# Kernel tuning notes

Measured on AMD Instinct MI355X. Metric: run time of the kernel, lower is better.

The kernel has to match this reference:

```python
import jax, jax.numpy as jnp
import numpy as np

B, S, E, H = 2, 2048, 1024, 16
HD = E // H


def setup_inputs() -> dict:
    key = jax.random.key(0)
    k1, k2, k3, k4 = jax.random.split(key, 4)
    x = jax.random.normal(k1, (B, S, E), dtype=jnp.float32)
    # nn.Linear(E, 3E, bias=False): weight shape (3E, E), y = x @ W.T
    w_qkv = jax.random.normal(k2, (3 * E, E), dtype=jnp.float32) * (E ** -0.5)
    w_proj = jax.random.normal(k3, (E, E), dtype=jnp.float32) * (E ** -0.5)
    b_proj = jax.random.normal(k4, (E,), dtype=jnp.float32) * 0.02
    return {"x": x, "w_qkv": w_qkv, "w_proj": w_proj, "b_proj": b_proj}


def reference(x, w_qkv, w_proj, b_proj):
    b, s, e = x.shape
    hd = e // H
    qkv = x @ w_qkv.T                                   # (B,S,3E)
    qkv = qkv.reshape(b, s, H, 3, hd)                   # matches view(B,S,H,3*hd).chunk(3,-1)
    q = jnp.transpose(qkv[..., 0, :], (0, 2, 1, 3))      # (B,H,S,hd)
    k = jnp.transpose(qkv[..., 1, :], (0, 2, 1, 3))
    v = jnp.transpose(qkv[..., 2, :], (0, 2, 1, 3))
    scale = hd ** -0.5
    scores = jnp.einsum('bhqd,bhkd->bhqk', q, k) * scale  # (B,H,S,S)
    causal = jnp.tril(jnp.ones((s, s), dtype=bool))
    scores = jnp.where(causal, scores, jnp.float32(-jnp.inf))
    probs = jax.nn.softmax(scores, axis=-1)
    out = jnp.einsum('bhqk,bhkd->bhqd', probs, v)        # (B,H,S,hd)
    out = jnp.transpose(out, (0, 2, 1, 3)).reshape(b, s, e)
    return out @ w_proj.T + b_proj
```

## Files before the change

kernel.cpp:

```cpp
#include <hip/hip_runtime.h>
#include <hip/hip_bf16.h>

#define B_    2
#define S_    2048
#define E_    1024
#define H_    16
#define HD_   64
#define M_    (B_ * S_)
#define QKVN  (3 * E_)

typedef __attribute__((ext_vector_type(8))) short  short8;
typedef __attribute__((ext_vector_type(4))) float  f32x4;

static __device__ __forceinline__ unsigned short f2bf(float f) {
  union { float f; unsigned int u; } c; c.f = f;
  unsigned int u = c.u;
  return (unsigned short)((u + 0x7fffu + ((u >> 16) & 1u)) >> 16);
}

static __device__ __forceinline__ void gload16(unsigned short* lds,
                                               const unsigned short* g) {
  __builtin_amdgcn_global_load_lds(
      (__attribute__((address_space(1))) void*)g,
      (__attribute__((address_space(3))) void*)lds, 16, 0, 0);
}

__global__ __launch_bounds__(256) void cvt_f32_to_bf16(
    const float* __restrict__ in, unsigned short* __restrict__ out, int n4) {
  int i = blockIdx.x * 256 + threadIdx.x;
  if (i < n4) {
    float4 v = reinterpret_cast<const float4*>(in)[i];
    ushort4 r;
    r.x = f2bf(v.x); r.y = f2bf(v.y); r.z = f2bf(v.z); r.w = f2bf(v.w);
    reinterpret_cast<ushort4*>(out)[i] = r;
  }
}

template <int BF16_OUT>
__global__ __launch_bounds__(256) void gemm_bt(
    const unsigned short* __restrict__ A, const unsigned short* __restrict__ Bt,
    void* __restrict__ Cout, const float* __restrict__ bias,
    int M, int N, int K, int ldc) {
  __shared__ alignas(16) unsigned short lds_a[128 * 64];
  __shared__ alignas(16) unsigned short lds_b[128 * 64];
  const int t  = threadIdx.x;
  const int w  = t >> 6, l = t & 63, g = l >> 4, lr = l & 15;
  const int bm = blockIdx.y * 128, bn = blockIdx.x * 128;
  const int wr = (w >> 1) * 64,  wc = (w & 1) * 64;

  f32x4 acc[4][4] = {};

  for (int k0 = 0; k0 < K; k0 += 64) {
    __syncthreads();
#pragma unroll
    for (int i = 0; i < 4; i++) {
      const int pass = w * 4 + i;
      const int r = pass * 8 + (l >> 3);
      const int c = (l & 7) ^ (r & 7);
      gload16(lds_a + pass * 512, A + (size_t)(bm + r) * K + k0 + c * 8);
      gload16(lds_b + pass * 512, Bt + (size_t)(bn + r) * K + k0 + c * 8);
    }
    __syncthreads();

    short8 af[4][2], bfr[4][2];
#pragma unroll
    for (int m = 0; m < 4; m++) {
      const int R = wr + m * 16 + lr;
#pragma unroll
      for (int kk = 0; kk < 2; kk++)
        af[m][kk] = *(const short8*)((const char*)lds_a +
            ((R * 128 + kk * 64 + g * 16) ^ ((R & 7) << 4)));
    }
#pragma unroll
    for (int n = 0; n < 4; n++) {
      const int R = wc + n * 16 + lr;
#pragma unroll
      for (int kk = 0; kk < 2; kk++)
        bfr[n][kk] = *(const short8*)((const char*)lds_b +
            ((R * 128 + kk * 64 + g * 16) ^ ((R & 7) << 4)));
    }
#pragma unroll
    for (int m = 0; m < 4; m++)
#pragma unroll
      for (int n = 0; n < 4; n++) {
        acc[m][n] = __builtin_amdgcn_mfma_f32_16x16x32_bf16(
            af[m][0], bfr[n][0], acc[m][n], 0, 0, 0);
        acc[m][n] = __builtin_amdgcn_mfma_f32_16x16x32_bf16(
            af[m][1], bfr[n][1], acc[m][n], 0, 0, 0);
      }
  }

#pragma unroll
  for (int m = 0; m < 4; m++)
#pragma unroll
    for (int n = 0; n < 4; n++)
#pragma unroll
      for (int j = 0; j < 4; j++) {
        const int row = bm + wr + m * 16 + g * 4 + j;
        const int col = bn + wc + n * 16 + lr;
        const float v = acc[m][n][j];
        if constexpr (BF16_OUT) {
          ((unsigned short*)Cout)[(size_t)row * ldc + col] = f2bf(v);
        } else {
          ((float*)Cout)[(size_t)row * ldc + col] = v + bias[col];
        }
      }
}

__global__ __launch_bounds__(256) void attn_fwd(
    const unsigned short* __restrict__ qkv, unsigned short* __restrict__ attn_out) {
  __shared__ alignas(16) unsigned short lds_k[64 * 64];
  __shared__ alignas(16) unsigned short lds_vt[64 * 64];
  __shared__ alignas(16) unsigned short lds_p[4][32 * 64];

  const int t = threadIdx.x;
  const int w = t >> 6, l = t & 63, g = l >> 4, lr = l & 15;
  const int bid = blockIdx.x;
  const int bh = bid & 31, b = bh >> 4, h = bh & 15;
  const int rr = bid >> 5;
  const int bx = (rr < 8) ? rr : 23 - rr;
  const int q0 = bx * 128;
  const int qw = q0 + w * 32;
  const unsigned short* base = qkv + (size_t)b * S_ * QKVN + h * (3 * HD_);

  short8 qf[2][2];
#pragma unroll
  for (int m = 0; m < 2; m++) {
    const unsigned short* qp = base + (size_t)(qw + m * 16 + lr) * QKVN + g * 8;
    qf[m][0] = *(const short8*)qp;
    qf[m][1] = *(const short8*)(qp + 32);
  }

  f32x4 o[2][4] = {};
  float m_r[2][4], l_r[2][4];
#pragma unroll
  for (int m = 0; m < 2; m++)
#pragma unroll
    for (int j = 0; j < 4; j++) { m_r[m][j] = -3.0e38f; l_r[m][j] = 0.f; }

  const int numt = 2 * bx + 2;
  for (int kt = 0; kt < numt; kt++) {
    const int k0 = kt * 64;
    __syncthreads();
#pragma unroll
    for (int p = 0; p < 2; p++) {
      const int r  = p * 32 + (t >> 3);
      const int kc = t & 7;
      const unsigned short* kp = base + (size_t)(k0 + r) * QKVN + HD_ + kc * 8;
      short8 kv8 = *(const short8*)kp;
      *(short8*)((char*)lds_k + ((r * 128 + kc * 16) ^ ((r & 7) << 4))) = kv8;
      short8 vv8 = *(const short8*)(kp + HD_);
#pragma unroll
      for (int j = 0; j < 8; j++) {
        const int d = kc * 8 + j;
        const int swz = ((d & 7) ^ ((d >> 3) & 7)) << 4;
        *(unsigned short*)((char*)lds_vt + ((d * 128 + r * 2) ^ swz)) =
            (unsigned short)vv8[j];
      }
    }
    __syncthreads();

    f32x4 s[2][4];
    __builtin_amdgcn_s_setprio(1);
#pragma unroll
    for (int n = 0; n < 4; n++) {
      const int R = n * 16 + lr;
      short8 b0 = *(const short8*)((const char*)lds_k +
          ((R * 128 + g * 16) ^ ((R & 7) << 4)));
      short8 b1 = *(const short8*)((const char*)lds_k +
          ((R * 128 + 64 + g * 16) ^ ((R & 7) << 4)));
#pragma unroll
      for (int m = 0; m < 2; m++) {
        f32x4 z = {};
        z = __builtin_amdgcn_mfma_f32_16x16x32_bf16(qf[m][0], b0, z, 0, 0, 0);
        z = __builtin_amdgcn_mfma_f32_16x16x32_bf16(qf[m][1], b1, z, 0, 0, 0);
        s[m][n] = z;
      }
    }
    __builtin_amdgcn_s_setprio(0);

    if (k0 + 63 > qw) {
#pragma unroll
      for (int m = 0; m < 2; m++)
#pragma unroll
        for (int n = 0; n < 4; n++) {
          const int kvc = k0 + n * 16 + lr;
#pragma unroll
          for (int j = 0; j < 4; j++) {
            const int qrow = qw + m * 16 + g * 4 + j;
            if (kvc > qrow) s[m][n][j] = -3.0e38f;
          }
        }
    }

#pragma unroll
    for (int m = 0; m < 2; m++) {
#pragma unroll
      for (int j = 0; j < 4; j++) {
        const float v0 = s[m][0][j] * 0.125f, v1 = s[m][1][j] * 0.125f;
        const float v2 = s[m][2][j] * 0.125f, v3 = s[m][3][j] * 0.125f;
        float mx = fmaxf(fmaxf(v0, v1), fmaxf(v2, v3));
#pragma unroll
        for (int dd = 8; dd; dd >>= 1) mx = fmaxf(mx, __shfl_xor(mx, dd, 16));
        const float mn = fmaxf(m_r[m][j], mx);
        const float c  = __expf(m_r[m][j] - mn);
        m_r[m][j] = mn;
        const float e0 = __expf(v0 - mn), e1 = __expf(v1 - mn);
        const float e2 = __expf(v2 - mn), e3 = __expf(v3 - mn);
        float sum = (e0 + e1) + (e2 + e3);
#pragma unroll
        for (int dd = 8; dd; dd >>= 1) sum += __shfl_xor(sum, dd, 16);
        l_r[m][j] = l_r[m][j] * c + sum;
#pragma unroll
        for (int dt = 0; dt < 4; dt++) o[m][dt][j] *= c;
        const int row = m * 16 + g * 4 + j;
        const int sw  = (row & 7) << 4;
        char* pb = (char*)lds_p[w];
        *(unsigned short*)(pb + ((row * 128 +      lr * 2) ^ sw)) = f2bf(e0);
        *(unsigned short*)(pb + ((row * 128 + 32 + lr * 2) ^ sw)) = f2bf(e1);
        *(unsigned short*)(pb + ((row * 128 + 64 + lr * 2) ^ sw)) = f2bf(e2);
        *(unsigned short*)(pb + ((row * 128 + 96 + lr * 2) ^ sw)) = f2bf(e3);
      }
    }
    __asm__ volatile("s_waitcnt lgkmcnt(0)" ::: "memory");

    __builtin_amdgcn_s_setprio(1);
#pragma unroll
    for (int m = 0; m < 2; m++) {
      const int prow = m * 16 + lr;
      const int psw  = (prow & 7) << 4;
      short8 pf0 = *(const short8*)((const char*)lds_p[w] +
          ((prow * 128 + g * 16) ^ psw));
      short8 pf1 = *(const short8*)((const char*)lds_p[w] +
          ((prow * 128 + 64 + g * 16) ^ psw));
#pragma unroll
      for (int dt = 0; dt < 4; dt++) {
        const int R = dt * 16 + lr;
        const int vsw = ((R & 7) ^ ((R >> 3) & 7)) << 4;
        short8 vf0 = *(const short8*)((const char*)lds_vt +
            ((R * 128 + g * 16) ^ vsw));
        short8 vf1 = *(const short8*)((const char*)lds_vt +
            ((R * 128 + 64 + g * 16) ^ vsw));
        o[m][dt] = __builtin_amdgcn_mfma_f32_16x16x32_bf16(pf0, vf0, o[m][dt], 0, 0, 0);
        o[m][dt] = __builtin_amdgcn_mfma_f32_16x16x32_bf16(pf1, vf1, o[m][dt], 0, 0, 0);
      }
    }
    __builtin_amdgcn_s_setprio(0);
  }

  unsigned short* outp = attn_out + (size_t)b * S_ * E_ + h * HD_;
#pragma unroll
  for (int m = 0; m < 2; m++)
#pragma unroll
    for (int j = 0; j < 4; j++) {
      const float inv = 1.0f / l_r[m][j];
      const int qrow = qw + m * 16 + g * 4 + j;
#pragma unroll
      for (int dt = 0; dt < 4; dt++)
        outp[(size_t)qrow * E_ + dt * 16 + lr] = f2bf(o[m][dt][j] * inv);
    }
}

extern "C" void kernel_launch(void* const* d_in, const int* in_sizes, int n_in,
                              void* d_out, int out_size, void* d_ws, size_t ws_size,
                              hipStream_t stream) {
  (void)in_sizes; (void)n_in; (void)out_size; (void)ws_size;
  const float* x      = (const float*)d_in[0];
  const float* w_qkv  = (const float*)d_in[1];
  const float* w_proj = (const float*)d_in[2];
  const float* b_proj = (const float*)d_in[3];
  float* out = (float*)d_out;

  unsigned short* x_bf     = (unsigned short*)d_ws;
  unsigned short* wqkv_bf  = x_bf    + (size_t)M_ * E_;
  unsigned short* wproj_bf = wqkv_bf + (size_t)QKVN * E_;
  unsigned short* qkv_bf   = wproj_bf + (size_t)E_ * E_;
  unsigned short* attn_bf  = qkv_bf  + (size_t)M_ * QKVN;

  int n4;
  n4 = M_ * E_ / 4;
  cvt_f32_to_bf16<<<(n4 + 255) / 256, 256, 0, stream>>>(x, x_bf, n4);
  n4 = QKVN * E_ / 4;
  cvt_f32_to_bf16<<<(n4 + 255) / 256, 256, 0, stream>>>(w_qkv, wqkv_bf, n4);
  n4 = E_ * E_ / 4;
  cvt_f32_to_bf16<<<(n4 + 255) / 256, 256, 0, stream>>>(w_proj, wproj_bf, n4);

  gemm_bt<1><<<dim3(QKVN / 128, M_ / 128), 256, 0, stream>>>(
      x_bf, wqkv_bf, (void*)qkv_bf, nullptr, M_, QKVN, E_, QKVN);

  attn_fwd<<<dim3(512), 256, 0, stream>>>(qkv_bf, attn_bf);

  gemm_bt<0><<<dim3(E_ / 128, M_ / 128), 256, 0, stream>>>(
      attn_bf, wproj_bf, (void*)out, b_proj, M_, E_, E_, E_);
}
```

Measured before the change: 244.1 us.

## Prefetch next K/V tile into registers, skip masked warp tiles, use DPP reductions

```diff
diff --git a/kernel.cpp b/kernel.cpp
--- a/kernel.cpp
+++ b/kernel.cpp
@@ -23,6 +23,29 @@
   __builtin_amdgcn_global_load_lds(
       (__attribute__((address_space(1))) void*)g,
       (__attribute__((address_space(3))) void*)lds, 16, 0, 0);
+}
+
+static __device__ __forceinline__ float dpp_max16(float x) {
+  x = fmaxf(x, __int_as_float(__builtin_amdgcn_update_dpp(
+          0, __float_as_int(x), 0xB1, 0xF, 0xF, true)));
+  x = fmaxf(x, __int_as_float(__builtin_amdgcn_update_dpp(
+          0, __float_as_int(x), 0x4E, 0xF, 0xF, true)));
+  x = fmaxf(x, __int_as_float(__builtin_amdgcn_update_dpp(
+          0, __float_as_int(x), 0x141, 0xF, 0xF, true)));
+  x = fmaxf(x, __int_as_float(__builtin_amdgcn_update_dpp(
+          0, __float_as_int(x), 0x140, 0xF, 0xF, true)));
+  return x;
+}
+static __device__ __forceinline__ float dpp_sum16(float x) {
+  x += __int_as_float(__builtin_amdgcn_update_dpp(
+          0, __float_as_int(x), 0xB1, 0xF, 0xF, true));
+  x += __int_as_float(__builtin_amdgcn_update_dpp(
+          0, __float_as_int(x), 0x4E, 0xF, 0xF, true));
+  x += __int_as_float(__builtin_amdgcn_update_dpp(
+          0, __float_as_int(x), 0x141, 0xF, 0xF, true));
+  x += __int_as_float(__builtin_amdgcn_update_dpp(
+          0, __float_as_int(x), 0x140, 0xF, 0xF, true));
+  return x;
 }
 
 __global__ __launch_bounds__(256) void cvt_f32_to_bf16(
@@ -114,7 +137,7 @@
   __shared__ alignas(16) unsigned short lds_p[4][32 * 64];
 
   const int t = threadIdx.x;
-  const int w = t >> 6, l = t & 63, g = l >> 4, lr = l & 15;
+  const int w = t >> 6, l = t & 63, g = (l >> 4) & 3, lr = l & 15;
   const int bid = blockIdx.x;
   const int bh = bid & 31, b = bh >> 4, h = bh & 15;
   const int rr = bid >> 5;
@@ -139,113 +162,129 @@
     for (int j = 0; j < 4; j++) { m_r[m][j] = -3.0e38f; l_r[m][j] = 0.f; }
 
   const int numt = 2 * bx + 2;
+  const int r_st = t >> 3;
+  const int kc   = t & 7;
+
+  short8 kreg[2], vreg[2];
+#pragma unroll
+  for (int p = 0; p < 2; p++) {
+    const unsigned short* kp =
+        base + (size_t)(p * 32 + r_st) * QKVN + HD_ + kc * 8;
+    kreg[p] = *(const short8*)kp;
+    vreg[p] = *(const short8*)(kp + HD_);
+  }
+
   for (int kt = 0; kt < numt; kt++) {
     const int k0 = kt * 64;
-    __syncthreads();
 #pragma unroll
     for (int p = 0; p < 2; p++) {
-      const int r  = p * 32 + (t >> 3);
-      const int kc = t & 7;
-      const unsigned short* kp = base + (size_t)(k0 + r) * QKVN + HD_ + kc * 8;
-      short8 kv8 = *(const short8*)kp;
-      *(short8*)((char*)lds_k + ((r * 128 + kc * 16) ^ ((r & 7) << 4))) = kv8;
-      short8 vv8 = *(const short8*)(kp + HD_);
+      const int r = p * 32 + r_st;
+      *(short8*)((char*)lds_k + ((r * 128 + kc * 16) ^ ((r & 7) << 4))) = kreg[p];
 #pragma unroll
       for (int j = 0; j < 8; j++) {
         const int d = kc * 8 + j;
         const int swz = ((d & 7) ^ ((d >> 3) & 7)) << 4;
         *(unsigned short*)((char*)lds_vt + ((d * 128 + r * 2) ^ swz)) =
-            (unsigned short)vv8[j];
+            (unsigned short)vreg[p][j];
+      }
+    }
+    if (kt + 1 < numt) {
+#pragma unroll
+      for (int p = 0; p < 2; p++) {
+        const unsigned short* kp =
+            base + (size_t)(k0 + 64 + p * 32 + r_st) * QKVN + HD_ + kc * 8;
+        kreg[p] = *(const short8*)kp;
+        vreg[p] = *(const short8*)(kp + HD_);
       }
     }
     __syncthreads();
 
-    f32x4 s[2][4];
-    __builtin_amdgcn_s_setprio(1);
-#pragma unroll
-    for (int n = 0; n < 4; n++) {
-      const int R = n * 16 + lr;
-      short8 b0 = *(const short8*)((const char*)lds_k +
-          ((R * 128 + g * 16) ^ ((R & 7) << 4)));
-      short8 b1 = *(const short8*)((const char*)lds_k +
-          ((R * 128 + 64 + g * 16) ^ ((R & 7) << 4)));
+    if (k0 <= qw + 31) {
+      f32x4 s[2][4];
+      __builtin_amdgcn_s_setprio(1);
+#pragma unroll
+      for (int n = 0; n < 4; n++) {
+        const int R = n * 16 + lr;
+        short8 b0 = *(const short8*)((const char*)lds_k +
+            ((R * 128 + g * 16) ^ ((R & 7) << 4)));
+        short8 b1 = *(const short8*)((const char*)lds_k +
+            ((R * 128 + 64 + g * 16) ^ ((R & 7) << 4)));
+#pragma unroll
+        for (int m = 0; m < 2; m++) {
+          f32x4 z = {};
+          z = __builtin_amdgcn_mfma_f32_16x16x32_bf16(qf[m][0], b0, z, 0, 0, 0);
+          z = __builtin_amdgcn_mfma_f32_16x16x32_bf16(qf[m][1], b1, z, 0, 0, 0);
+          s[m][n] = z;
+        }
+      }
+      __builtin_amdgcn_s_setprio(0);
+
+      if (k0 + 63 > qw) {
+#pragma unroll
+        for (int m = 0; m < 2; m++)
+#pragma unroll
+          for (int n = 0; n < 4; n++) {
+            const int kvc = k0 + n * 16 + lr;
+#pragma unroll
+            for (int j = 0; j < 4; j++) {
+              const int qrow = qw + m * 16 + g * 4 + j;
+              if (kvc > qrow) s[m][n][j] = -3.0e38f;
+            }
+          }
+      }
+
 #pragma unroll
       for (int m = 0; m < 2; m++) {
-        f32x4 z = {};
-        z = __builtin_amdgcn_mfma_f32_16x16x32_bf16(qf[m][0], b0, z, 0, 0, 0);
-        z = __builtin_amdgcn_mfma_f32_16x16x32_bf16(qf[m][1], b1, z, 0, 0, 0);
-        s[m][n] = z;
-      }
-    }
-    __builtin_amdgcn_s_setprio(0);
-
-    if (k0 + 63 > qw) {
-#pragma unroll
-      for (int m = 0; m < 2; m++)
-#pragma unroll
-        for (int n = 0; n < 4; n++) {
-          const int kvc = k0 + n * 16 + lr;
-#pragma unroll
-          for (int j = 0; j < 4; j++) {
-            const int qrow = qw + m * 16 + g * 4 + j;
-            if (kvc > qrow) s[m][n][j] = -3.0e38f;
-          }
+#pragma unroll
+        for (int j = 0; j < 4; j++) {
+          const float v0 = s[m][0][j] * 0.125f, v1 = s[m][1][j] * 0.125f;
+          const float v2 = s[m][2][j] * 0.125f, v3 = s[m][3][j] * 0.125f;
+          float mx = dpp_max16(fmaxf(fmaxf(v0, v1), fmaxf(v2, v3)));
+          const float mn = fmaxf(m_r[m][j], mx);
+          const float c  = __expf(m_r[m][j] - mn);
+          m_r[m][j] = mn;
+          const float e0 = __expf(v0 - mn), e1 = __expf(v1 - mn);
+          const float e2 = __expf(v2 - mn), e3 = __expf(v3 - mn);
+          const float sum = dpp_sum16((e0 + e1) + (e2 + e3));
+          l_r[m][j] = l_r[m][j] * c + sum;
+#pragma unroll
+          for (int dt = 0; dt < 4; dt++) o[m][dt][j] *= c;
+          const int row = m * 16 + g * 4 + j;
+          const int sw  = (row & 7) << 4;
+          char* pb = (char*)lds_p[w];
+          *(unsigned short*)(pb + ((row * 128 +      lr * 2) ^ sw)) = f2bf(e0);
+          *(unsigned short*)(pb + ((row * 128 + 32 + lr * 2) ^ sw)) = f2bf(e1);
+          *(unsigned short*)(pb + ((row * 128 + 64 + lr * 2) ^ sw)) = f2bf(e2);
+          *(unsigned short*)(pb + ((row * 128 + 96 + lr * 2) ^ sw)) = f2bf(e3);
         }
-    }
-
-#pragma unroll
-    for (int m = 0; m < 2; m++) {
-#pragma unroll
-      for (int j = 0; j < 4; j++) {
-        const float v0 = s[m][0][j] * 0.125f, v1 = s[m][1][j] * 0.125f;
-        const float v2 = s[m][2][j] * 0.125f, v3 = s[m][3][j] * 0.125f;
-        float mx = fmaxf(fmaxf(v0, v1), fmaxf(v2, v3));
-#pragma unroll
-        for (int dd = 8; dd; dd >>= 1) mx = fmaxf(mx, __shfl_xor(mx, dd, 16));
-        const float mn = fmaxf(m_r[m][j], mx);
-        const float c  = __expf(m_r[m][j] - mn);
-        m_r[m][j] = mn;
-        const float e0 = __expf(v0 - mn), e1 = __expf(v1 - mn);
-        const float e2 = __expf(v2 - mn), e3 = __expf(v3 - mn);
-        float sum = (e0 + e1) + (e2 + e3);
-#pragma unroll
-        for (int dd = 8; dd; dd >>= 1) sum += __shfl_xor(sum, dd, 16);
-        l_r[m][j] = l_r[m][j] * c + sum;
-#pragma unroll
-        for (int dt = 0; dt < 4; dt++) o[m][dt][j] *= c;
-        const int row = m * 16 + g * 4 + j;
-        const int sw  = (row & 7) << 4;
-        char* pb = (char*)lds_p[w];
-        *(unsigned short*)(pb + ((row * 128 +      lr * 2) ^ sw)) = f2bf(e0);
-        *(unsigned short*)(pb + ((row * 128 + 32 + lr * 2) ^ sw)) = f2bf(e1);
-        *(unsigned short*)(pb + ((row * 128 + 64 + lr * 2) ^ sw)) = f2bf(e2);
-        *(unsigned short*)(pb + ((row * 128 + 96 + lr * 2) ^ sw)) = f2bf(e3);
-      }
-    }
-    __asm__ volatile("s_waitcnt lgkmcnt(0)" ::: "memory");
-
-    __builtin_amdgcn_s_setprio(1);
-#pragma unroll
-    for (int m = 0; m < 2; m++) {
-      const int prow = m * 16 + lr;
-      const int psw  = (prow & 7) << 4;
-      short8 pf0 = *(const short8*)((const char*)lds_p[w] +
-          ((prow * 128 + g * 16) ^ psw));
-      short8 pf1 = *(const short8*)((const char*)lds_p[w] +
-          ((prow * 128 + 64 + g * 16) ^ psw));
-#pragma unroll
-      for (int dt = 0; dt < 4; dt++) {
-        const int R = dt * 16 + lr;
-        const int vsw = ((R & 7) ^ ((R >> 3) & 7)) << 4;
-        short8 vf0 = *(const short8*)((const char*)lds_vt +
-            ((R * 128 + g * 16) ^ vsw));
-        short8 vf1 = *(const short8*)((const char*)lds_vt +
-            ((R * 128 + 64 + g * 16) ^ vsw));
-        o[m][dt] = __builtin_amdgcn_mfma_f32_16x16x32_bf16(pf0, vf0, o[m][dt], 0, 0, 0);
-        o[m][dt] = __builtin_amdgcn_mfma_f32_16x16x32_bf16(pf1, vf1, o[m][dt], 0, 0, 0);
-      }
-    }
-    __builtin_amdgcn_s_setprio(0);
+      }
+      __asm__ volatile("s_waitcnt lgkmcnt(0)" ::: "memory");
+
+      __builtin_amdgcn_s_setprio(1);
+#pragma unroll
+      for (int m = 0; m < 2; m++) {
+        const int prow = m * 16 + lr;
+        const int psw  = (prow & 7) << 4;
+        short8 pf0 = *(const short8*)((const char*)lds_p[w] +
+            ((prow * 128 + g * 16) ^ psw));
+        short8 pf1 = *(const short8*)((const char*)lds_p[w] +
+            ((prow * 128 + 64 + g * 16) ^ psw));
+#pragma unroll
+        for (int dt = 0; dt < 4; dt++) {
+          const int R = dt * 16 + lr;
+          const int vsw = ((R & 7) ^ ((R >> 3) & 7)) << 4;
+          short8 vf0 = *(const short8*)((const char*)lds_vt +
+              ((R * 128 + g * 16) ^ vsw));
+          short8 vf1 = *(const short8*)((const char*)lds_vt +
+              ((R * 128 + 64 + g * 16) ^ vsw));
+          o[m][dt] = __builtin_amdgcn_mfma_f32_16x16x32_bf16(pf0, vf0, o[m][dt], 0, 0, 0);
+          o[m][dt] = __builtin_amdgcn_mfma_f32_16x16x32_bf16(pf1, vf1, o[m][dt], 0, 0, 0);
+        }
+      }
+      __builtin_amdgcn_s_setprio(0);
+    }
+
+    __syncthreads();
   }
 
   unsigned short* outp = attn_out + (size_t)b * S_ * E_ + h * HD_;
```

New measurement: 226.6 us. 1.08x faster.
